# Performance work log

Hardware: AMD Instinct MI355X
Metric: run time of the kernel (lower is better)

## Reference

```python
import jax, jax.numpy as jnp
import numpy as np

# static sizes (see shape_source)
IN_SIZE = 50000
M = 3            # n_modalities
N0 = 40960       # layer-0 sampled source nodes
N1 = 16384       # layer-0 dst == layer-1 src
B = 4096         # batch (final dst nodes)
HEADS = 4
DIM = 64
HD = HEADS * DIM # 256, integration_size
DEG0, DEG1 = 16, 16
E0, E1 = N1 * DEG0, B * DEG1
NEG_SLOPE = 0.2  # GATConv default negative_slope


def gat_conv(x_src, e_src, e_dst, n_dst, W, att, bias):
    """PyG GATConv with bipartite input (x, None): attention uses only alpha_l.
    x_src: [Ns, HD]; W: [HD, HD]; att: [1, H, C]; returns [n_dst, HD]."""
    x_l = (x_src @ W.T).reshape(-1, HEADS, DIM)            # [Ns, H, C]
    alpha_l = (x_l * att).sum(-1)                          # [Ns, H]
    logits = jax.nn.leaky_relu(alpha_l[e_src], NEG_SLOPE)  # [E, H]
    m = jax.ops.segment_max(logits, e_dst, num_segments=n_dst)
    m = jnp.where(jnp.isfinite(m), m, 0.0)                 # guard empty segments
    e = jnp.exp(logits - m[e_dst])
    denom = jax.ops.segment_sum(e, e_dst, num_segments=n_dst)
    a = e / (denom[e_dst] + 1e-16)                         # edge softmax per dst
    msg = x_l[e_src] * a[:, :, None]                       # [E, H, C]
    out = jax.ops.segment_sum(msg, e_dst, num_segments=n_dst)
    return out.reshape(n_dst, HD) + bias


def interp(scales_param, mask, key):
    """Interp module, evaluate=False, idxs = range(M)."""
    scales = jax.nn.softmax(scales_param, axis=-1)         # [1, M]
    rm = jax.random.randint(key, mask.shape, 0, 2).astype(jnp.float32)
    rm = rm + (1.0 / (1.0 + rm.sum(-1)) ** 20)[:, None]
    rm = rm + (1.0 / (mask.sum(-1) ** 20))[:, None]
    rm = jax.lax.stop_gradient(jnp.floor(rm))              # .int().float()
    rm = rm / (rm + 1e-10)
    m = mask * rm
    m = jax.nn.softmax(m + (1.0 - m) * (-1e10), axis=-1)   # [B, M]
    return scales, m


def setup_inputs() -> dict:
    key = jax.random.key(0)
    ks = jax.random.split(key, 12)
    s = 0.05
    return {
        "masks": jnp.ones((B, M), jnp.float32),
        "n_ids": jax.random.randint(ks[0], (M, N0), 0, IN_SIZE, dtype=jnp.int32),
        "e0_src": jax.random.randint(ks[1], (M, E0), 0, N0, dtype=jnp.int32),
        "e0_dst": jnp.repeat(jnp.arange(N1, dtype=jnp.int32), DEG0),
        "e1_src": jax.random.randint(ks[2], (M, E1), 0, N1, dtype=jnp.int32),
        "e1_dst": jnp.repeat(jnp.arange(B, dtype=jnp.int32), DEG1),
        "pre_W": jax.random.normal(ks[3], (M, HD, IN_SIZE), jnp.float32) * s,
        "pre_b": jax.random.normal(ks[4], (M, HD), jnp.float32) * s,
        "gat_W": jax.random.normal(ks[5], (M, HD, HD), jnp.float32) * s,
        "gat_att": jax.random.normal(ks[6], (M, 1, HEADS, DIM), jnp.float32) * s,
        "gat_b": jax.random.normal(ks[7], (M, HD), jnp.float32) * s,
        "scales_param": jnp.full((1, M), 1.0 / M, jnp.float32),
        "emb_W": jax.random.normal(ks[8], (128, HD), jnp.float32) * s,
        "emb_b": jax.random.normal(ks[9], (128,), jnp.float32) * s,
    }


def reference(masks, n_ids, e0_src, e0_dst, e1_src, e1_dst,
              pre_W, pre_b, gat_W, gat_att, gat_b,
              scales_param, emb_W, emb_b):
    scales, interp_masks = interp(scales_param, masks, jax.random.key(42))
    x_mod = jnp.zeros((B, HD), dtype=masks.dtype)
    for i in range(M):  # small fixed modality loop (structurally distinct params)
        # one-hot(n_id) @ W.T + b  ==  gather of columns of W (same math)
        x = jnp.take(pre_W[i], n_ids[i], axis=1).T + pre_b[i]        # [N0, HD]
        g0 = gat_conv(x, e0_src[i], e0_dst, N1, gat_W[i], gat_att[i], gat_b[i])
        g1 = gat_conv(g0, e1_src[i], e1_dst, B, gat_W[i], gat_att[i], gat_b[i])
        # x_store_layer = [g0[:B] (sliced), g0[:B] (x_pre), g1]; x = sum + g1
        xm = 2.0 * g0[:B] + 2.0 * g1                                  # [B, HD]
        xm = scales[:, i] * interp_masks[:, i].reshape(-1, 1) * xm
        x_mod = x_mod + xm
    emb = x_mod @ emb_W.T + emb_b                                     # [B, 128]
    dot = emb @ emb.T                                                 # [B, B]
    return dot, emb, scales
```

## Files before the change

kernel.cpp:

```cpp
#include <hip/hip_runtime.h>
#include <hip/hip_bf16.h>
#include <cstdint>

#define IN_SZ 50000
#define PADC  50048
#define NM 3
#define N0 40960
#define N1 16384
#define NB 4096
#define HD 256
#define DEG 16
#define E0 (N1*DEG)
#define E1 (NB*DEG)

using short8v = __attribute__((ext_vector_type(8))) short;
using floatx4 = __attribute__((ext_vector_type(4))) float;
typedef unsigned short ushort_t;

__device__ __forceinline__ ushort_t f2bf(float f){
  uint32_t u = __float_as_uint(f);
  uint32_t r = u + 0x7FFFu + ((u>>16)&1u);
  return (ushort_t)(r>>16);
}
__device__ __forceinline__ float bf2f(ushort_t h){
  return __uint_as_float(((uint32_t)h)<<16);
}
__device__ __forceinline__ void gload_lds16(const void* g, void* l){
  __builtin_amdgcn_global_load_lds(
      (const __attribute__((address_space(1))) void*)g,
      (__attribute__((address_space(3))) void*)l, 16, 0, 0);
}

__device__ __forceinline__ uint32_t rotl32(uint32_t x, uint32_t d){ return (x<<d)|(x>>(32u-d)); }

__device__ void tf2x32(uint32_t k0, uint32_t k1, uint32_t c0, uint32_t c1,
                       uint32_t& y0, uint32_t& y1)
{
  uint32_t ks2 = k0 ^ k1 ^ 0x1BD11BDAu;
  uint32_t x0 = c0 + k0, x1 = c1 + k1;
#define R4(a,b,c,d) \
  x0+=x1; x1=rotl32(x1,a); x1^=x0; \
  x0+=x1; x1=rotl32(x1,b); x1^=x0; \
  x0+=x1; x1=rotl32(x1,c); x1^=x0; \
  x0+=x1; x1=rotl32(x1,d); x1^=x0;
  R4(13,15,26,6)  x0+=k1;  x1+=ks2+1u;
  R4(17,29,16,24) x0+=ks2; x1+=k0+2u;
  R4(13,15,26,6)  x0+=k0;  x1+=k1+3u;
  R4(17,29,16,24) x0+=k1;  x1+=ks2+4u;
  R4(13,15,26,6)  x0+=ks2; x1+=k0+5u;
#undef R4
  y0=x0; y1=x1;
}

__global__ __launch_bounds__(256) void prep_k(
    const float* __restrict__ masks, const float* __restrict__ sp,
    float* __restrict__ coef, float* __restrict__ scales_out,
    const float* __restrict__ emb_W, float* __restrict__ wT,
    const float* __restrict__ gat_W, ushort_t* __restrict__ gWhi, ushort_t* __restrict__ gWlo,
    const float* __restrict__ pre_b, const float* __restrict__ gat_att,
    const float* __restrict__ gat_b, float* __restrict__ bsum, float* __restrict__ batt,
    float* __restrict__ watt)
{
  int blk = blockIdx.x;
  int t = threadIdx.x;
  if (blk < 16){
    int b = blk*256 + t;
    float s0=sp[0], s1=sp[1], s2=sp[2];
    float mx = fmaxf(s0,fmaxf(s1,s2));
    float e0=expf(s0-mx), e1=expf(s1-mx), e2=expf(s2-mx);
    float inv = 1.f/(e0+e1+e2);
    float sc[3] = {e0*inv, e1*inv, e2*inv};
    if (b == 0){ scales_out[0]=sc[0]; scales_out[1]=sc[1]; scales_out[2]=sc[2]; }
    uint32_t bits[3];
    uint32_t K0,K1, t0,t1;
    tf2x32(0u,42u,0u,1u,K0,K1);
    for (int i=0;i<3;i++){
      uint32_t idx = (uint32_t)(b*3+i);
      tf2x32(K0,K1,0u,idx,t0,t1);
      bits[i] = (t0 ^ t1) & 1u;
    }
    float mk[3] = {masks[b*3+0], masks[b*3+1], masks[b*3+2]};
    float msum = mk[0]+mk[1]+mk[2];
    float rs = (float)(bits[0]+bits[1]+bits[2]);
    float add = powf(1.f/(1.f+rs), 20.f) + powf(1.f/msum, 20.f);
    float lg[3]; float lmax = -1e30f;
    for (int i=0;i<3;i++){
      float rm = floorf((float)bits[i] + add);
      rm = rm/(rm+1e-10f);
      float mm = mk[i]*rm;
      lg[i] = mm + (1.f-mm)*(-1e10f);
      lmax = fmaxf(lmax, lg[i]);
    }
    float es[3], ssum=0.f;
    for (int i=0;i<3;i++){ es[i]=expf(lg[i]-lmax); ssum+=es[i]; }
    for (int i=0;i<3;i++) coef[b*3+i] = sc[i]*es[i]/ssum;
  } else if (blk < 144){
    int g = (blk-16)*256 + t;
    int j = g >> 8, k = g & 255;
    wT[k*128 + j] = emb_W[g];
  } else if (blk < 912){
    int g = (blk-144)*256 + t;
    float v = gat_W[g];
    ushort_t h = f2bf(v);
    gWhi[g] = h;
    gWlo[g] = f2bf(v - bf2f(h));
  } else if (blk < 915){
    int i = blk - 912, o = t;
    const float* W = gat_W + (size_t)i*HD*HD + (size_t)o*HD;
    const float* b = pre_b + i*HD;
    float s = 0.f;
    for (int k=0;k<HD;k++) s = fmaf(b[k], W[k], s);
    bsum[i*HD + o] = s + gat_b[i*HD + o];
    __shared__ float red[256];
    red[o] = s * gat_att[i*HD + o];
    __syncthreads();
    if (o < 4){
      float p = 0.f;
      for (int j=0;j<64;j++) p += red[o*64 + j];
      batt[i*4 + o] = p;
    }
  } else {
    int idx = blk - 915;
    int i = idx >> 2, h = idx & 3;
    int k = t;
    float s = 0.f;
    for (int o=0;o<64;o++){
      int oo = h*64 + o;
      s = fmaf(gat_W[(size_t)i*HD*HD + (size_t)oo*HD + k], gat_att[i*HD + oo], s);
    }
    watt[(size_t)i*1024 + k*4 + h] = s;
  }
}

__global__ __launch_bounds__(256) void transpA_k(
    const float* __restrict__ Wb, const float* __restrict__ watt_b,
    const float* __restrict__ batt, ushort_t* __restrict__ WT_b,
    float* __restrict__ alphaG_b)
{
  int i = blockIdx.y;
  int c0 = blockIdx.x * 64;
  const float* W = Wb + (size_t)i*HD*IN_SZ;
  ushort_t* WT = WT_b + (size_t)i*(size_t)PADC*HD;
  float* alphaG = alphaG_b + (size_t)i*(size_t)PADC*4;

  __shared__ uint32_t tile[256*33];
  __shared__ float wl[1024];
  int t = threadIdx.x;
  {
    const float* wg = watt_b + (size_t)i*1024;
#pragma unroll
    for (int j=0;j<4;j++) wl[j*256 + t] = wg[j*256 + t];
  }
#pragma unroll
  for (int it=0; it<16; it++){
    int lin = it*256 + t;
    int k = lin >> 4, quad = lin & 15;
    int cb = c0 + quad*4;
    float4 f;
    if (cb + 3 < IN_SZ){
      f = *reinterpret_cast<const float4*>(&W[(size_t)k*IN_SZ + cb]);
    } else {
      float tmp[4] = {0.f,0.f,0.f,0.f};
#pragma unroll
      for (int e=0;e<4;e++) if (cb+e < IN_SZ) tmp[e] = W[(size_t)k*IN_SZ + cb+e];
      f = make_float4(tmp[0],tmp[1],tmp[2],tmp[3]);
    }
    tile[k*33 + quad*2]     = (uint32_t)f2bf(f.x) | ((uint32_t)f2bf(f.y)<<16);
    tile[k*33 + quad*2 + 1] = (uint32_t)f2bf(f.z) | ((uint32_t)f2bf(f.w)<<16);
  }
  __syncthreads();

  int c = t>>2, kp = t&3, half = c&1, cu = c>>1;
  float p0=0.f,p1=0.f,p2=0.f,p3=0.f;
  uint32_t ou[32];
#pragma unroll
  for (int j=0;j<32;j++){
    int k0 = kp*64 + 2*j;
    uint32_t ua = tile[k0*33 + cu];
    uint32_t ub = tile[(k0+1)*33 + cu];
    ushort_t va = half ? (ushort_t)(ua>>16) : (ushort_t)(ua & 0xffffu);
    ushort_t vb = half ? (ushort_t)(ub>>16) : (ushort_t)(ub & 0xffffu);
    ou[j] = (uint32_t)va | ((uint32_t)vb<<16);
    float fa = bf2f(va), fb = bf2f(vb);
    p0 = fmaf(fa, wl[k0*4+0], p0); p1 = fmaf(fa, wl[k0*4+1], p1);
    p2 = fmaf(fa, wl[k0*4+2], p2); p3 = fmaf(fa, wl[k0*4+3], p3);
    p0 = fmaf(fb, wl[(k0+1)*4+0], p0); p1 = fmaf(fb, wl[(k0+1)*4+1], p1);
    p2 = fmaf(fb, wl[(k0+1)*4+2], p2); p3 = fmaf(fb, wl[(k0+1)*4+3], p3);
  }
  uint32_t* orow = reinterpret_cast<uint32_t*>(WT + (size_t)(c0+c)*HD + kp*64);
#pragma unroll
  for (int j=0;j<8;j++){
    uint4 v = make_uint4(ou[4*j], ou[4*j+1], ou[4*j+2], ou[4*j+3]);
    *reinterpret_cast<uint4*>(orow + j*4) = v;
  }
  p0 += __shfl_xor(p0, 1, 64); p0 += __shfl_xor(p0, 2, 64);
  p1 += __shfl_xor(p1, 1, 64); p1 += __shfl_xor(p1, 2, 64);
  p2 += __shfl_xor(p2, 1, 64); p2 += __shfl_xor(p2, 2, 64);
  p3 += __shfl_xor(p3, 1, 64); p3 += __shfl_xor(p3, 2, 64);
  float pv = (kp==0) ? p0 : (kp==1) ? p1 : (kp==2) ? p2 : p3;
  pv += batt[i*4 + kp];
  alphaG[(size_t)(c0+c)*4 + kp] = pv > 0.f ? pv : 0.2f*pv;
}

__global__ __launch_bounds__(128) void gat_msg0w(
    const ushort_t* __restrict__ WT_b, const float* __restrict__ alphaG_b,
    const int* __restrict__ n_ids, const int* __restrict__ esrc_b,
    ushort_t* __restrict__ agg_b)
{
  int i = blockIdx.y, d = blockIdx.x, t = threadIdx.x;
  const ushort_t* WT = WT_b + (size_t)i*(size_t)PADC*HD;
  const float* alphaG = alphaG_b + (size_t)i*(size_t)PADC*4;
  __shared__ int src[16];
  __shared__ float aw[16][4];
  if (t < 16) src[t] = n_ids[(size_t)i*N0 + esrc_b[(size_t)i*E0 + d*16 + t]];
  __syncthreads();
  if (t < 64){
    int e = t&15, h = t>>4;
    float l = alphaG[(size_t)src[e]*4 + h];
    float m = l;
#pragma unroll
    for (int off=1; off<16; off<<=1) m = fmaxf(m, __shfl_xor(m, off, 64));
    float ex = expf(l - m);
    float s = ex;
#pragma unroll
    for (int off=1; off<16; off<<=1) s += __shfl_xor(s, off, 64);
    aw[e][h] = ex / (s + 1e-16f);
  }
  __syncthreads();
  int h = t >> 5;
  float a0=0.f, a1=0.f;
#pragma unroll
  for (int e=0;e<16;e++){
    uint32_t u = *reinterpret_cast<const uint32_t*>(WT + (size_t)src[e]*HD + 2*t);
    float w = aw[e][h];
    a0 = fmaf(w, bf2f((ushort_t)(u & 0xffffu)), a0);
    a1 = fmaf(w, bf2f((ushort_t)(u >> 16)), a1);
  }
  uint32_t pk = (uint32_t)f2bf(a0) | ((uint32_t)f2bf(a1)<<16);
  reinterpret_cast<uint32_t*>(agg_b + ((size_t)i*N1 + d)*HD)[t] = pk;
}

template<bool BIASMODE>
__global__ __launch_bounds__(256) void gemm2(
    const ushort_t* __restrict__ A_b, size_t a_stride,
    const ushort_t* __restrict__ Whi_b, const ushort_t* __restrict__ Wlo_b,
    ushort_t* __restrict__ C_b, size_t c_stride,
    const float* __restrict__ att_b, float* __restrict__ alpha_b, size_t al_stride,
    const float* __restrict__ bias_b)
{
  int i = blockIdx.z;
  int bn0 = blockIdx.x * 128;
  int brow = blockIdx.y * 128;
  const ushort_t* A = A_b + (size_t)i*a_stride;
  const ushort_t* Whi = Whi_b + (size_t)i*HD*HD;
  const ushort_t* Wlo = Wlo_b + (size_t)i*HD*HD;
  ushort_t* C = C_b + (size_t)i*c_stride;

  __shared__ __align__(16) ushort_t smem[2][24*512];
  int t = threadIdx.x, wave = t>>6, lane = t&63;
  int l15 = lane&15, kq = lane>>4;

  int row0 = brow + wave*16 + l15;
  int row1 = brow + (wave+4)*16 + l15;

  const ushort_t* gsrc[6];
  gsrc[0] = A + (size_t)row0*HD + kq*8;
  gsrc[1] = A + (size_t)row1*HD + kq*8;
#pragma unroll
  for (int j=2;j<6;j++){
    int idx = wave + 4*(j-2);
    int ct = idx>>1, h = idx&1;
    const ushort_t* W = h ? Wlo : Whi;
    gsrc[j] = W + (size_t)(bn0 + ct*16 + l15)*HD + kq*8;
  }

  floatx4 acc[4][4];
#pragma unroll
  for (int r=0;r<4;r++)
#pragma unroll
    for (int c=0;c<4;c++) acc[r][c] = (floatx4){0.f,0.f,0.f,0.f};

  int wm = wave>>1, wn = wave&1;

#pragma unroll
  for (int j=0;j<6;j++)
    gload_lds16(gsrc[j], &smem[0][(wave + 4*j)*512] + lane*8);
  __syncthreads();

  for (int cc=0; cc<8; cc++){
    int buf = cc & 1;
    if (cc < 7){
      int k0 = (cc+1)*32;
#pragma unroll
      for (int j=0;j<6;j++)
        gload_lds16(gsrc[j] + k0, &smem[buf^1][(wave + 4*j)*512] + lane*8);
    }
    short8v a[4];
#pragma unroll
    for (int r=0;r<4;r++)
      a[r] = *reinterpret_cast<const short8v*>(&smem[buf][(wm*4+r)*512 + lane*8]);
#pragma unroll
    for (int c=0;c<4;c++){
      int ct = wn*4+c;
      short8v bh = *reinterpret_cast<const short8v*>(&smem[buf][(8+ct*2)*512 + lane*8]);
      short8v bl = *reinterpret_cast<const short8v*>(&smem[buf][(9+ct*2)*512 + lane*8]);
#pragma unroll
      for (int r=0;r<4;r++){
        acc[r][c] = __builtin_amdgcn_mfma_f32_16x16x32_bf16(a[r], bh, acc[r][c], 0,0,0);
        acc[r][c] = __builtin_amdgcn_mfma_f32_16x16x32_bf16(a[r], bl, acc[r][c], 0,0,0);
      }
    }
    __syncthreads();
  }

  float attv[4];
#pragma unroll
  for (int c=0;c<4;c++){
    int col = bn0 + (wn*4+c)*16 + l15;
    if constexpr (BIASMODE) attv[c] = bias_b[i*HD + col];
    else                    attv[c] = att_b[(size_t)i*HD + col];
  }
  int head = (bn0>>6) + wn;
#pragma unroll
  for (int r=0;r<4;r++){
    int rowb = brow + wm*64 + r*16 + kq*4;
#pragma unroll
    for (int j=0;j<4;j++){
      size_t rw = (size_t)(rowb + j)*HD;
#pragma unroll
      for (int c=0;c<4;c++){
        float v = acc[r][c][j];
        if constexpr (BIASMODE) v += attv[c];
        C[rw + bn0 + (wn*4+c)*16 + l15] = f2bf(v);
      }
    }
    if constexpr (!BIASMODE){
#pragma unroll
      for (int j=0;j<4;j++){
        float p = acc[r][0][j]*attv[0] + acc[r][1][j]*attv[1]
                + acc[r][2][j]*attv[2] + acc[r][3][j]*attv[3];
        p += __shfl_xor(p, 1, 64);
        p += __shfl_xor(p, 2, 64);
        p += __shfl_xor(p, 4, 64);
        p += __shfl_xor(p, 8, 64);
        if (l15 == 0){
          float lg = p > 0.f ? p : 0.2f*p;
          alpha_b[(size_t)i*al_stride + (size_t)(rowb + j)*4 + head] = lg;
        }
      }
    }
  }
}

__global__ __launch_bounds__(128) void gat_msg1(
    const ushort_t* __restrict__ xl1hi, const float* __restrict__ alpha1,
    const int* __restrict__ e1src, const float* __restrict__ gat_b,
    const uint32_t* __restrict__ g0_u, const float* __restrict__ coef,
    float* __restrict__ xmod)
{
  int d = blockIdx.x, t = threadIdx.x;
  __shared__ int src[16];
  __shared__ float aw[16][4];
  float o0 = 0.f, o1 = 0.f;
  for (int i=0;i<NM;i++){
    if (t < 16) src[t] = e1src[(size_t)i*E1 + d*16 + t];
    __syncthreads();
    if (t < 64){
      int e = t&15, h = t>>4;
      float l = alpha1[((size_t)i*N1 + src[e])*4 + h];
      float m = l;
#pragma unroll
      for (int off=1; off<16; off<<=1) m = fmaxf(m, __shfl_xor(m, off, 64));
      float ex = expf(l - m);
      float s = ex;
#pragma unroll
      for (int off=1; off<16; off<<=1) s += __shfl_xor(s, off, 64);
      aw[e][h] = ex / (s + 1e-16f);
    }
    __syncthreads();
    const ushort_t* xl = xl1hi + (size_t)i*N1*HD;
    int h = t >> 5;
    float a0=0.f, a1=0.f;
#pragma unroll
    for (int e=0;e<16;e++){
      uint32_t u = *reinterpret_cast<const uint32_t*>(xl + (size_t)src[e]*HD + 2*t);
      float w = aw[e][h];
      a0 = fmaf(w, bf2f((ushort_t)(u & 0xffffu)), a0);
      a1 = fmaf(w, bf2f((ushort_t)(u >> 16)), a1);
    }
    uint32_t gh = g0_u[((size_t)i*N1 + d)*128 + t];
    float g00 = bf2f((ushort_t)(gh & 0xffffu));
    float g01 = bf2f((ushort_t)(gh >> 16));
    const float* bias = gat_b + i*HD;
    float cv = coef[d*3 + i];
    o0 += cv*(2.f*g00 + 2.f*(a0 + bias[2*t]));
    o1 += cv*(2.f*g01 + 2.f*(a1 + bias[2*t+1]));
    __syncthreads();
  }
  *reinterpret_cast<float2*>(&xmod[(size_t)d*HD + 2*t]) = make_float2(o0, o1);
}

__global__ __launch_bounds__(256) void emb_gemm(
  const float* __restrict__ xmod, const float* __restrict__ wT,
  const float* __restrict__ eb, float* __restrict__ emb,
  ushort_t* __restrict__ ehi, ushort_t* __restrict__ elo)
{
  __shared__ float xs[32][260];
  int t = threadIdx.x;
  int brow = blockIdx.x * 32;
#pragma unroll
  for (int j=0;j<8;j++){
    int linear = j*256+t;
    int row = linear >> 6;
    int kq = linear & 63;
    float4 f = *reinterpret_cast<const float4*>(&xmod[(size_t)(brow+row)*256 + kq*4]);
    xs[row][kq*4+0]=f.x; xs[row][kq*4+1]=f.y; xs[row][kq*4+2]=f.z; xs[row][kq*4+3]=f.w;
  }
  __syncthreads();
  int tj = t & 127, th = t >> 7;
  float acc[16];
#pragma unroll
  for(int r=0;r<16;r++) acc[r]=0.f;
  for (int k=0;k<256;k++){
    float w = wT[k*128 + tj];
#pragma unroll
    for (int r=0;r<16;r++) acc[r] = fmaf(xs[th*16+r][k], w, acc[r]);
  }
  float bias = eb[tj];
#pragma unroll
  for (int r=0;r<16;r++){
    size_t idx = (size_t)(brow+th*16+r)*128 + tj;
    float v = acc[r] + bias;
    emb[idx] = v;
    ushort_t hb = f2bf(v);
    ehi[idx] = hb;
    elo[idx] = f2bf(v - bf2f(hb));
  }
}

__global__ __launch_bounds__(256) void dot_mfma(
    const ushort_t* __restrict__ Ehi, const ushort_t* __restrict__ Elo,
    float* __restrict__ dot)
{
  __shared__ __align__(16) ushort_t lb[2][16384];
  int t = threadIdx.x, wave = t>>6, lane = t&63;
  int arow0 = blockIdx.y*128, brow0 = blockIdx.x*128;
  {
    const ushort_t* srcp = (t<128) ? Ehi : Elo;
    ushort_t* dstb = lb[(t<128)?0:1];
    int o = t & 127;
    const ushort_t* rp = srcp + (size_t)(brow0+o)*128;
#pragma unroll
    for (int g=0; g<16; g++){
      short8v v = *reinterpret_cast<const short8v*>(rp + g*8);
      int c = g>>2, grp = g&3;
      int lidx = c*4096 + (o>>4)*512 + ((grp<<4)|(o&15))*8;
      *reinterpret_cast<short8v*>(&dstb[lidx]) = v;
    }
  }
  __syncthreads();

  floatx4 acc[2][8];
#pragma unroll
  for (int rt=0;rt<2;rt++)
#pragma unroll
    for (int ot=0;ot<8;ot++) acc[rt][ot] = (floatx4){0.f,0.f,0.f,0.f};

  int ar0 = arow0 + wave*32 + (lane&15);
  int ar1 = ar0 + 16;
  int koff = (lane>>4)*8;
#pragma unroll
  for (int c=0;c<4;c++){
    short8v ah0 = *reinterpret_cast<const short8v*>(Ehi + (size_t)ar0*128 + c*32 + koff);
    short8v ah1 = *reinterpret_cast<const short8v*>(Ehi + (size_t)ar1*128 + c*32 + koff);
    short8v al0 = *reinterpret_cast<const short8v*>(Elo + (size_t)ar0*128 + c*32 + koff);
    short8v al1 = *reinterpret_cast<const short8v*>(Elo + (size_t)ar1*128 + c*32 + koff);
#pragma unroll
    for (int ot=0;ot<8;ot++){
      short8v bh = *reinterpret_cast<const short8v*>(&lb[0][c*4096 + ot*512 + lane*8]);
      short8v bl = *reinterpret_cast<const short8v*>(&lb[1][c*4096 + ot*512 + lane*8]);
      acc[0][ot] = __builtin_amdgcn_mfma_f32_16x16x32_bf16(ah0, bh, acc[0][ot], 0,0,0);
      acc[0][ot] = __builtin_amdgcn_mfma_f32_16x16x32_bf16(ah0, bl, acc[0][ot], 0,0,0);
      acc[0][ot] = __builtin_amdgcn_mfma_f32_16x16x32_bf16(al0, bh, acc[0][ot], 0,0,0);
      acc[1][ot] = __builtin_amdgcn_mfma_f32_16x16x32_bf16(ah1, bh, acc[1][ot], 0,0,0);
      acc[1][ot] = __builtin_amdgcn_mfma_f32_16x16x32_bf16(ah1, bl, acc[1][ot], 0,0,0);
      acc[1][ot] = __builtin_amdgcn_mfma_f32_16x16x32_bf16(al1, bh, acc[1][ot], 0,0,0);
    }
  }
#pragma unroll
  for (int rt=0;rt<2;rt++){
    int rb = arow0 + wave*32 + rt*16 + (lane>>4)*4;
#pragma unroll
    for (int r=0;r<4;r++)
#pragma unroll
      for (int ot=0;ot<8;ot++)
        dot[(size_t)(rb+r)*4096 + brow0 + ot*16 + (lane&15)] = acc[rt][ot][r];
  }
}

extern "C" void kernel_launch(void* const* d_in, const int* in_sizes, int n_in,
                              void* d_out, int out_size, void* d_ws, size_t ws_size,
                              hipStream_t stream) {
  (void)in_sizes; (void)n_in; (void)out_size; (void)ws_size;
  const float* masks   = (const float*)d_in[0];
  const int*   n_ids   = (const int*)d_in[1];
  const int*   e0_src  = (const int*)d_in[2];
  const int*   e1_src  = (const int*)d_in[4];
  const float* pre_W   = (const float*)d_in[6];
  const float* pre_b   = (const float*)d_in[7];
  const float* gat_W   = (const float*)d_in[8];
  const float* gat_att = (const float*)d_in[9];
  const float* gat_b   = (const float*)d_in[10];
  const float* sp      = (const float*)d_in[11];
  const float* emb_W   = (const float*)d_in[12];
  const float* emb_b   = (const float*)d_in[13];

  float* out = (float*)d_out;
  float* dot = out;
  float* emb = out + (size_t)NB*NB;
  float* scales_out = emb + (size_t)NB*128;

  char* p = (char*)d_ws;
  auto alloc = [&](size_t bytes)->char*{ char* r = p; p += (bytes + 255) & ~(size_t)255; return r; };
  ushort_t* WT    = (ushort_t*)alloc((size_t)NM*PADC*HD*2);
  float*    alphG = (float*)alloc((size_t)NM*PADC*4*4);
  ushort_t* agg   = (ushort_t*)alloc((size_t)NM*N1*HD*2);
  uint32_t* g0u   = (uint32_t*)alloc((size_t)NM*N1*HD*2);
  ushort_t* xl1hi = (ushort_t*)alloc((size_t)NM*N1*HD*2);
  float*    alph1 = (float*)alloc((size_t)NM*N1*4*4);
  float*    xmod  = (float*)alloc((size_t)NB*HD*4);
  float*    coef  = (float*)alloc((size_t)NB*3*4);
  float*    wT    = (float*)alloc((size_t)HD*128*4);
  ushort_t* gWhi  = (ushort_t*)alloc((size_t)NM*HD*HD*2);
  ushort_t* gWlo  = (ushort_t*)alloc((size_t)NM*HD*HD*2);
  float*    bsum  = (float*)alloc((size_t)NM*HD*4);
  float*    batt  = (float*)alloc((size_t)NM*4*4);
  float*    watt  = (float*)alloc((size_t)NM*1024*4);
  ushort_t* ehi   = (ushort_t*)alloc((size_t)NB*128*2);
  ushort_t* elo   = (ushort_t*)alloc((size_t)NB*128*2);

  prep_k<<<927, 256, 0, stream>>>(masks, sp, coef, scales_out, emb_W, wT,
                                  gat_W, gWhi, gWlo, pre_b, gat_att, gat_b,
                                  bsum, batt, watt);
  transpA_k<<<dim3(PADC/64, NM), 256, 0, stream>>>(pre_W, watt, batt, WT, alphG);
  gat_msg0w<<<dim3(N1, NM), 128, 0, stream>>>(WT, alphG, n_ids, e0_src, agg);
  gemm2<true><<<dim3(2, N1/128, NM), 256, 0, stream>>>(
      agg, (size_t)N1*HD, gWhi, gWlo,
      (ushort_t*)g0u, (size_t)N1*HD, nullptr, nullptr, 0, bsum);
  gemm2<false><<<dim3(2, N1/128, NM), 256, 0, stream>>>(
      (const ushort_t*)g0u, (size_t)N1*HD, gWhi, gWlo,
      xl1hi, (size_t)N1*HD, gat_att, alph1, (size_t)N1*4, nullptr);
  gat_msg1<<<NB, 128, 0, stream>>>(xl1hi, alph1, e1_src, gat_b, g0u, coef, xmod);
  emb_gemm<<<NB/32, 256, 0, stream>>>(xmod, wT, emb_b, emb, ehi, elo);
  dot_mfma<<<dim3(32,32), 256, 0, stream>>>(ehi, elo, dot);
}
```

Before: 274.7 us.

## Retile pre_W transpose into 256-column by 64-k blocks with split alpha partials

```diff
diff --git a/kernel.cpp b/kernel.cpp
--- a/kernel.cpp
+++ b/kernel.cpp
@@ -132,91 +132,81 @@
   }
 }
 
-__global__ __launch_bounds__(256) void transpA_k(
+__global__ __launch_bounds__(256) void transpB_k(
     const float* __restrict__ Wb, const float* __restrict__ watt_b,
-    const float* __restrict__ batt, ushort_t* __restrict__ WT_b,
-    float* __restrict__ alphaG_b)
-{
-  int i = blockIdx.y;
-  int c0 = blockIdx.x * 64;
+    ushort_t* __restrict__ WT_b, float* __restrict__ alphG4_b)
+{
+  int i = blockIdx.z;
+  int kq = blockIdx.y;
+  int c0 = blockIdx.x * 256;
   const float* W = Wb + (size_t)i*HD*IN_SZ;
   ushort_t* WT = WT_b + (size_t)i*(size_t)PADC*HD;
-  float* alphaG = alphaG_b + (size_t)i*(size_t)PADC*4;
-
-  __shared__ uint32_t tile[256*33];
-  __shared__ float wl[1024];
+  float* alphG4 = alphG4_b + (size_t)(i*4 + kq)*(size_t)PADC*4;
+
+  __shared__ uint32_t tile[64*129];
+  __shared__ float wl[256];
   int t = threadIdx.x;
-  {
-    const float* wg = watt_b + (size_t)i*1024;
-#pragma unroll
-    for (int j=0;j<4;j++) wl[j*256 + t] = wg[j*256 + t];
-  }
+  wl[t] = watt_b[(size_t)i*1024 + (size_t)kq*256 + t];
+
 #pragma unroll
   for (int it=0; it<16; it++){
     int lin = it*256 + t;
-    int k = lin >> 4, quad = lin & 15;
+    int kl = lin >> 6, quad = lin & 63;
     int cb = c0 + quad*4;
-    float4 f;
-    if (cb + 3 < IN_SZ){
-      f = *reinterpret_cast<const float4*>(&W[(size_t)k*IN_SZ + cb]);
-    } else {
-      float tmp[4] = {0.f,0.f,0.f,0.f};
-#pragma unroll
-      for (int e=0;e<4;e++) if (cb+e < IN_SZ) tmp[e] = W[(size_t)k*IN_SZ + cb+e];
-      f = make_float4(tmp[0],tmp[1],tmp[2],tmp[3]);
-    }
-    tile[k*33 + quad*2]     = (uint32_t)f2bf(f.x) | ((uint32_t)f2bf(f.y)<<16);
-    tile[k*33 + quad*2 + 1] = (uint32_t)f2bf(f.z) | ((uint32_t)f2bf(f.w)<<16);
+    if (cb > IN_SZ-4) cb = IN_SZ-4;
+    float4 f = *reinterpret_cast<const float4*>(&W[(size_t)(kq*64+kl)*IN_SZ + cb]);
+    tile[kl*129 + quad*2]     = (uint32_t)f2bf(f.x) | ((uint32_t)f2bf(f.y)<<16);
+    tile[kl*129 + quad*2 + 1] = (uint32_t)f2bf(f.z) | ((uint32_t)f2bf(f.w)<<16);
   }
   __syncthreads();
 
-  int c = t>>2, kp = t&3, half = c&1, cu = c>>1;
+  int c = c0 + t, half = t & 1, cu = t >> 1;
   float p0=0.f,p1=0.f,p2=0.f,p3=0.f;
   uint32_t ou[32];
 #pragma unroll
   for (int j=0;j<32;j++){
-    int k0 = kp*64 + 2*j;
-    uint32_t ua = tile[k0*33 + cu];
-    uint32_t ub = tile[(k0+1)*33 + cu];
+    uint32_t ua = tile[(2*j)*129 + cu];
+    uint32_t ub = tile[(2*j+1)*129 + cu];
     ushort_t va = half ? (ushort_t)(ua>>16) : (ushort_t)(ua & 0xffffu);
     ushort_t vb = half ? (ushort_t)(ub>>16) : (ushort_t)(ub & 0xffffu);
     ou[j] = (uint32_t)va | ((uint32_t)vb<<16);
     float fa = bf2f(va), fb = bf2f(vb);
-    p0 = fmaf(fa, wl[k0*4+0], p0); p1 = fmaf(fa, wl[k0*4+1], p1);
-    p2 = fmaf(fa, wl[k0*4+2], p2); p3 = fmaf(fa, wl[k0*4+3], p3);
-    p0 = fmaf(fb, wl[(k0+1)*4+0], p0); p1 = fmaf(fb, wl[(k0+1)*4+1], p1);
-    p2 = fmaf(fb, wl[(k0+1)*4+2], p2); p3 = fmaf(fb, wl[(k0+1)*4+3], p3);
-  }
-  uint32_t* orow = reinterpret_cast<uint32_t*>(WT + (size_t)(c0+c)*HD + kp*64);
-#pragma unroll
-  for (int j=0;j<8;j++){
-    uint4 v = make_uint4(ou[4*j], ou[4*j+1], ou[4*j+2], ou[4*j+3]);
-    *reinterpret_cast<uint4*>(orow + j*4) = v;
-  }
-  p0 += __shfl_xor(p0, 1, 64); p0 += __shfl_xor(p0, 2, 64);
-  p1 += __shfl_xor(p1, 1, 64); p1 += __shfl_xor(p1, 2, 64);
-  p2 += __shfl_xor(p2, 1, 64); p2 += __shfl_xor(p2, 2, 64);
-  p3 += __shfl_xor(p3, 1, 64); p3 += __shfl_xor(p3, 2, 64);
-  float pv = (kp==0) ? p0 : (kp==1) ? p1 : (kp==2) ? p2 : p3;
-  pv += batt[i*4 + kp];
-  alphaG[(size_t)(c0+c)*4 + kp] = pv > 0.f ? pv : 0.2f*pv;
+    p0 = fmaf(fa, wl[(2*j)*4+0], p0); p1 = fmaf(fa, wl[(2*j)*4+1], p1);
+    p2 = fmaf(fa, wl[(2*j)*4+2], p2); p3 = fmaf(fa, wl[(2*j)*4+3], p3);
+    p0 = fmaf(fb, wl[(2*j+1)*4+0], p0); p1 = fmaf(fb, wl[(2*j+1)*4+1], p1);
+    p2 = fmaf(fb, wl[(2*j+1)*4+2], p2); p3 = fmaf(fb, wl[(2*j+1)*4+3], p3);
+  }
+  if (c < PADC){
+    uint32_t* orow = reinterpret_cast<uint32_t*>(WT + (size_t)c*HD + kq*64);
+#pragma unroll
+    for (int j=0;j<8;j++){
+      uint4 v = make_uint4(ou[4*j], ou[4*j+1], ou[4*j+2], ou[4*j+3]);
+      *reinterpret_cast<uint4*>(orow + j*4) = v;
+    }
+    *reinterpret_cast<float4*>(&alphG4[(size_t)c*4]) = make_float4(p0,p1,p2,p3);
+  }
 }
 
 __global__ __launch_bounds__(128) void gat_msg0w(
-    const ushort_t* __restrict__ WT_b, const float* __restrict__ alphaG_b,
+    const ushort_t* __restrict__ WT_b, const float* __restrict__ alphG4_b,
+    const float* __restrict__ batt,
     const int* __restrict__ n_ids, const int* __restrict__ esrc_b,
     ushort_t* __restrict__ agg_b)
 {
   int i = blockIdx.y, d = blockIdx.x, t = threadIdx.x;
   const ushort_t* WT = WT_b + (size_t)i*(size_t)PADC*HD;
-  const float* alphaG = alphaG_b + (size_t)i*(size_t)PADC*4;
+  const float* alphG4 = alphG4_b + (size_t)(i*4)*(size_t)PADC*4;
   __shared__ int src[16];
   __shared__ float aw[16][4];
   if (t < 16) src[t] = n_ids[(size_t)i*N0 + esrc_b[(size_t)i*E0 + d*16 + t]];
   __syncthreads();
   if (t < 64){
     int e = t&15, h = t>>4;
-    float l = alphaG[(size_t)src[e]*4 + h];
+    size_t so = (size_t)src[e]*4 + h;
+    float v = alphG4[so] + alphG4[(size_t)PADC*4 + so]
+            + alphG4[(size_t)PADC*8 + so] + alphG4[(size_t)PADC*12 + so];
+    v += batt[i*4 + h];
+    float l = v > 0.f ? v : 0.2f*v;
     float m = l;
 #pragma unroll
     for (int off=1; off<16; off<<=1) m = fmaxf(m, __shfl_xor(m, off, 64));
@@ -523,7 +513,7 @@
   char* p = (char*)d_ws;
   auto alloc = [&](size_t bytes)->char*{ char* r = p; p += (bytes + 255) & ~(size_t)255; return r; };
   ushort_t* WT    = (ushort_t*)alloc((size_t)NM*PADC*HD*2);
-  float*    alphG = (float*)alloc((size_t)NM*PADC*4*4);
+  float*    alphG4= (float*)alloc((size_t)NM*4*PADC*4*4);
   ushort_t* agg   = (ushort_t*)alloc((size_t)NM*N1*HD*2);
   uint32_t* g0u   = (uint32_t*)alloc((size_t)NM*N1*HD*2);
   ushort_t* xl1hi = (ushort_t*)alloc((size_t)NM*N1*HD*2);
@@ -542,8 +532,8 @@
   prep_k<<<927, 256, 0, stream>>>(masks, sp, coef, scales_out, emb_W, wT,
                                   gat_W, gWhi, gWlo, pre_b, gat_att, gat_b,
                                   bsum, batt, watt);
-  transpA_k<<<dim3(PADC/64, NM), 256, 0, stream>>>(pre_W, watt, batt, WT, alphG);
-  gat_msg0w<<<dim3(N1, NM), 128, 0, stream>>>(WT, alphG, n_ids, e0_src, agg);
+  transpB_k<<<dim3((PADC+255)/256, 4, NM), 256, 0, stream>>>(pre_W, watt, WT, alphG4);
+  gat_msg0w<<<dim3(N1, NM), 128, 0, stream>>>(WT, alphG4, batt, n_ids, e0_src, agg);
   gemm2<true><<<dim3(2, N1/128, NM), 256, 0, stream>>>(
       agg, (size_t)N1*HD, gWhi, gWlo,
       (ushort_t*)g0u, (size_t)N1*HD, nullptr, nullptr, 0, bsum);
```

After: 268.7 us. 1.02x faster.
